# Kernel tuning notes

Measured on AMD Instinct MI355X. Metric: run time of the kernel, lower is better.

The kernel has to match this reference:

```python
import jax, jax.numpy as jnp
import numpy as np

ALPHA = 0.2  # LeakyReLU negative slope


def setup_inputs() -> dict:
    key = jax.random.key(0)
    k_x, k_w, k_a = jax.random.split(key, 3)
    B, N, F_in = 4, 2048, 128
    H, nhid = 4, 32  # out_channel=128, nheads=4
    x = jax.random.normal(k_x, (B, N, F_in), dtype=jnp.float32)
    # per-head projection and attention vector, xavier-ish scale
    W = jax.random.normal(k_w, (H, F_in, nhid), dtype=jnp.float32) * (1.414 * np.sqrt(2.0 / (F_in + nhid))) / np.sqrt(3.0) * np.sqrt(3.0)
    a = jax.random.normal(k_a, (H, 2 * nhid), dtype=jnp.float32) * (1.414 * np.sqrt(2.0 / (2 * nhid + 1)))
    return {"x": x, "W": W, "a": a}


def reference(x, W, a):
    # x: [B,N,F_in], W: [H,F_in,d], a: [H,2d]
    H = W.shape[0]
    d = W.shape[2]
    B, N, _ = x.shape
    Wh = jnp.einsum('bni,hij->bhnj', x, W)          # [B,H,N,d]
    a1 = a[:, :d]                                    # [H,d]
    a2 = a[:, d:]                                    # [H,d]
    Wh1 = jnp.einsum('bhnd,hd->bhn', Wh, a1)         # [B,H,N]
    Wh2 = jnp.einsum('bhnd,hd->bhn', Wh, a2)         # [B,H,N]
    e = Wh1[:, :, :, None] + Wh2[:, :, None, :]      # [B,H,N,N]
    e = jnp.where(e > 0, e, ALPHA * e)               # LeakyReLU
    attn = jax.nn.softmax(e, axis=-1)                # softmax over source nodes
    h = jnp.einsum('bhij,bhjd->bhid', attn, Wh)      # [B,H,N,d]
    h = jax.nn.elu(h)
    # concat heads along feature dim: [B,N,H*d]
    out = jnp.transpose(h, (0, 2, 1, 3)).reshape(B, N, H * d)
    return out
```

## Files before the change

### kernel.cpp

```cpp
#include <hip/hip_runtime.h>


#define LOG2E 1.4426950408889634f
constexpr int Nn = 2048, Fin = 128, Dd = 32;

typedef _Float16 half8 __attribute__((ext_vector_type(8)));
typedef _Float16 half4v __attribute__((ext_vector_type(4)));
typedef float f32x4 __attribute__((ext_vector_type(4)));

__global__ __launch_bounds__(256) void k1_wh(
    const float* __restrict__ x, const float* __restrict__ W,
    const float* __restrict__ a, _Float16* __restrict__ whT,
    float* __restrict__ sArr, float* __restrict__ tArr) {
  int blk = blockIdx.x;
  int bh = blk >> 5, tile = blk & 31;
  int b = bh >> 2, h = bh & 3;
  int tid = threadIdx.x, w = tid >> 6, lane = tid & 63;
  int q = lane >> 4, m = lane & 15;
  int rowbase = tile * 64 + w * 16;

  const float* Wq = W + h * Fin * Dd;
  const float* xb = x + (size_t)(b * Nn + rowbase + m) * Fin;

  f32x4 acc[2];
  acc[0] = (f32x4){0.f, 0.f, 0.f, 0.f};
  acc[1] = (f32x4){0.f, 0.f, 0.f, 0.f};

#pragma unroll
  for (int kt = 0; kt < 4; ++kt) {
    float4 x0 = *(const float4*)(xb + kt * 32 + q * 8);
    float4 x1 = *(const float4*)(xb + kt * 32 + q * 8 + 4);
    float xv[8] = {x0.x, x0.y, x0.z, x0.w, x1.x, x1.y, x1.z, x1.w};
    half8 Ah, Al;
#pragma unroll
    for (int j = 0; j < 8; ++j) {
      _Float16 hi = (_Float16)xv[j];
      Ah[j] = hi;
      Al[j] = (_Float16)(xv[j] - (float)hi);
    }
#pragma unroll
    for (int nt = 0; nt < 2; ++nt) {
      half8 Bh, Bl;
#pragma unroll
      for (int j = 0; j < 8; ++j) {
        float wv = Wq[(kt * 32 + q * 8 + j) * Dd + nt * 16 + m];
        _Float16 hi = (_Float16)wv;
        Bh[j] = hi;
        Bl[j] = (_Float16)(wv - (float)hi);
      }
      acc[nt] = __builtin_amdgcn_mfma_f32_16x16x32_f16(Ah, Bh, acc[nt], 0, 0, 0);
      acc[nt] = __builtin_amdgcn_mfma_f32_16x16x32_f16(Al, Bh, acc[nt], 0, 0, 0);
      acc[nt] = __builtin_amdgcn_mfma_f32_16x16x32_f16(Ah, Bl, acc[nt], 0, 0, 0);
    }
  }

#pragma unroll
  for (int nt = 0; nt < 2; ++nt) {
    int d = nt * 16 + m;
    half4v h4;
#pragma unroll
    for (int r = 0; r < 4; ++r) h4[r] = (_Float16)acc[nt][r];
    *(half4v*)(whT + (size_t)(bh * Dd + d) * Nn + rowbase + q * 4) = h4;
  }

  const float* ah = a + h * 2 * Dd;
  float a1m0 = ah[m], a1m1 = ah[16 + m];
  float a2m0 = ah[Dd + m], a2m1 = ah[Dd + 16 + m];
#pragma unroll
  for (int r = 0; r < 4; ++r) {
    float ps = acc[0][r] * a1m0 + acc[1][r] * a1m1;
    float pt = acc[0][r] * a2m0 + acc[1][r] * a2m1;
#pragma unroll
    for (int off = 1; off < 16; off <<= 1) {
      ps += __shfl_xor(ps, off);
      pt += __shfl_xor(pt, off);
    }
    if (m == 0) {
      sArr[bh * Nn + rowbase + q * 4 + r] = ps;
      tArr[bh * Nn + rowbase + q * 4 + r] = pt;
    }
  }
}

__global__ __launch_bounds__(256) void k3_attn(
    const _Float16* __restrict__ whT, const float* __restrict__ sArr,
    const float* __restrict__ tArr, float* __restrict__ out) {
  __shared__ float smem[4 * 64 * 33 + 256];
  float* Ut = smem;
  float* Vt = smem + 2048;
  float* red = smem + 4096;

  int blk = blockIdx.x;
  int bh = blk >> 5, tile = blk & 31;
  int b = bh >> 2, h = bh & 3;
  int tid = threadIdx.x, w = tid >> 6, lane = tid & 63;
  int q = lane >> 4, m = lane & 15;

  float mx = -1e30f;
  for (int i = tid; i < Nn; i += 256) {
    float t = tArr[bh * Nn + i];
    Ut[i] = LOG2E * t;
    Vt[i] = (0.2f * LOG2E) * t;
    mx = fmaxf(mx, t);
  }
  red[tid] = mx;
  __syncthreads();
  for (int ss = 128; ss > 0; ss >>= 1) {
    if (tid < ss) red[tid] = fmaxf(red[tid], red[tid + ss]);
    __syncthreads();
  }
  float T = red[0];

  float Ar[4], Cr[4];
#pragma unroll
  for (int t = 0; t < 4; ++t) {
    float s = sArr[bh * Nn + tile * 64 + t * 16 + m];
    float e = s + T;
    float mm = fmaxf(e, 0.2f * e);
    Ar[t] = LOG2E * (s - mm);
    Cr[t] = LOG2E * (0.2f * s - mm);
  }

  f32x4 acc[4][2];
#pragma unroll
  for (int t = 0; t < 4; ++t) {
    acc[t][0] = (f32x4){0.f, 0.f, 0.f, 0.f};
    acc[t][1] = (f32x4){0.f, 0.f, 0.f, 0.f};
  }
  float den[4] = {0.f, 0.f, 0.f, 0.f};

  const _Float16* wb = whT + (size_t)bh * Dd * Nn;

  for (int s = 0; s < 16; ++s) {
    int jb = w * 512 + s * 32;
    half8 B0 = *(const half8*)(wb + (size_t)m * Nn + jb + q * 8);
    half8 B1 = *(const half8*)(wb + (size_t)(16 + m) * Nn + jb + q * 8);
    float uu[8], vv[8];
    *(float4*)&uu[0] = *(const float4*)&Ut[jb + q * 8];
    *(float4*)&uu[4] = *(const float4*)&Ut[jb + q * 8 + 4];
    *(float4*)&vv[0] = *(const float4*)&Vt[jb + q * 8];
    *(float4*)&vv[4] = *(const float4*)&Vt[jb + q * 8 + 4];

#pragma unroll
    for (int t = 0; t < 4; ++t) {
      half8 P;
      float ds = 0.f;
#pragma unroll
      for (int k = 0; k < 8; ++k) {
        float p = __builtin_amdgcn_exp2f(fmaxf(Ar[t] + uu[k], Cr[t] + vv[k]));
        ds += p;
        P[k] = (_Float16)p;
      }
      den[t] += ds;
      acc[t][0] = __builtin_amdgcn_mfma_f32_16x16x32_f16(P, B0, acc[t][0], 0, 0, 0);
      acc[t][1] = __builtin_amdgcn_mfma_f32_16x16x32_f16(P, B1, acc[t][1], 0, 0, 0);
    }
  }

#pragma unroll
  for (int t = 0; t < 4; ++t) {
    den[t] += __shfl_xor(den[t], 16);
    den[t] += __shfl_xor(den[t], 32);
  }
  __syncthreads();
  float* redN = smem;
  float* redD = smem + 4 * 64 * 33;
#pragma unroll
  for (int t = 0; t < 4; ++t) {
#pragma unroll
    for (int dh = 0; dh < 2; ++dh)
#pragma unroll
      for (int r = 0; r < 4; ++r)
        redN[(w * 64 + t * 16 + q * 4 + r) * 33 + dh * 16 + m] = acc[t][dh][r];
    if (q == 0) redD[w * 64 + t * 16 + m] = den[t];
  }
  __syncthreads();
  {
    int rl = tid >> 2, dg = (tid & 3) * 8;
    float num[8];
#pragma unroll
    for (int i = 0; i < 8; ++i)
      num[i] = redN[(0 * 64 + rl) * 33 + dg + i] + redN[(1 * 64 + rl) * 33 + dg + i] +
               redN[(2 * 64 + rl) * 33 + dg + i] + redN[(3 * 64 + rl) * 33 + dg + i];
    float dt = redD[rl] + redD[64 + rl] + redD[128 + rl] + redD[192 + rl];
    float rd = 1.0f / dt;
    float* orow = out + (size_t)(b * Nn + tile * 64 + rl) * (4 * Dd) + h * Dd + dg;
#pragma unroll
    for (int i = 0; i < 8; ++i) {
      float hv = num[i] * rd;
      num[i] = hv > 0.f ? hv : (__builtin_amdgcn_exp2f(hv * LOG2E) - 1.0f);
    }
    *(float4*)orow = make_float4(num[0], num[1], num[2], num[3]);
    *((float4*)orow + 1) = make_float4(num[4], num[5], num[6], num[7]);
  }
}

extern "C" void kernel_launch(void* const* d_in, const int* in_sizes, int n_in,
                              void* d_out, int out_size, void* d_ws, size_t ws_size,
                              hipStream_t stream) {
  const float* x = (const float*)d_in[0];
  const float* W = (const float*)d_in[1];
  const float* a = (const float*)d_in[2];
  float* out = (float*)d_out;

  float* wsf = (float*)d_ws;
  float* sArr = wsf;
  float* tArr = sArr + 32768;
  _Float16* whT = (_Float16*)(tArr + 32768);

  k1_wh<<<dim3(512), dim3(256), 0, stream>>>(x, W, a, whT, sArr, tArr);
  k3_attn<<<dim3(512), dim3(256), 0, stream>>>(whT, sArr, tArr, out);
}
```

Before: 84.31 us.

## Factor attention exponentials into per-row and per-column terms with packed fp16 math

Rewrites the leaky-ReLU softmax weights as max(alpha_i*E_j, beta_i*F_j). E_j and F_j are exponentials of the shifted source scores, computed once per block and stored in LDS as fp16. The inner loop then does packed half2 multiplies and max plus fdot2 accumulation instead of one exp2 per element. This removes most transcendental work from the hot loop and halves LDS traffic, at the cost of fp16 precision in the products and possible underflow for large score ranges.

```diff
diff --git a/kernel.cpp b/kernel.cpp
--- a/kernel.cpp
+++ b/kernel.cpp
@@ -6,7 +6,10 @@
 
 typedef _Float16 half8 __attribute__((ext_vector_type(8)));
 typedef _Float16 half4v __attribute__((ext_vector_type(4)));
+typedef _Float16 half2v __attribute__((ext_vector_type(2)));
 typedef float f32x4 __attribute__((ext_vector_type(4)));
+
+union H8 { half2v h2[4]; half8 h8; };
 
 __global__ __launch_bounds__(256) void k1_wh(
     const float* __restrict__ x, const float* __restrict__ W,
@@ -86,9 +89,9 @@
     const _Float16* __restrict__ whT, const float* __restrict__ sArr,
     const float* __restrict__ tArr, float* __restrict__ out) {
   __shared__ float smem[4 * 64 * 33 + 256];
-  float* Ut = smem;
-  float* Vt = smem + 2048;
-  float* red = smem + 4096;
+  _Float16* Ef = (_Float16*)smem;
+  _Float16* Ff = (_Float16*)(smem + 1024);
+  float* red = smem + 2048;
 
   int blk = blockIdx.x;
   int bh = blk >> 5, tile = blk & 31;
@@ -96,12 +99,12 @@
   int tid = threadIdx.x, w = tid >> 6, lane = tid & 63;
   int q = lane >> 4, m = lane & 15;
 
+  float tv[8];
   float mx = -1e30f;
-  for (int i = tid; i < Nn; i += 256) {
-    float t = tArr[bh * Nn + i];
-    Ut[i] = LOG2E * t;
-    Vt[i] = (0.2f * LOG2E) * t;
-    mx = fmaxf(mx, t);
+#pragma unroll
+  for (int k = 0; k < 8; ++k) {
+    tv[k] = tArr[bh * Nn + tid + k * 256];
+    mx = fmaxf(mx, tv[k]);
   }
   red[tid] = mx;
   __syncthreads();
@@ -110,16 +113,25 @@
     __syncthreads();
   }
   float T = red[0];
-
-  float Ar[4], Cr[4];
-#pragma unroll
-  for (int t = 0; t < 4; ++t) {
-    float s = sArr[bh * Nn + tile * 64 + t * 16 + m];
-    float e = s + T;
-    float mm = fmaxf(e, 0.2f * e);
-    Ar[t] = LOG2E * (s - mm);
-    Cr[t] = LOG2E * (0.2f * s - mm);
-  }
+  __syncthreads();
+#pragma unroll
+  for (int k = 0; k < 8; ++k) {
+    float dt = tv[k] - T;
+    Ef[tid + k * 256] = (_Float16)__builtin_amdgcn_exp2f(LOG2E * dt);
+    Ff[tid + k * 256] = (_Float16)__builtin_amdgcn_exp2f(0.2f * LOG2E * dt);
+  }
+
+  half2v aa[4], bb[4];
+#pragma unroll
+  for (int t = 0; t < 4; ++t) {
+    float es = sArr[bh * Nn + tile * 64 + t * 16 + m] + T;
+    float al = __builtin_amdgcn_exp2f(0.8f * LOG2E * fminf(es, 0.f));
+    float be = __builtin_amdgcn_exp2f(-0.8f * LOG2E * fmaxf(es, 0.f));
+    _Float16 ah_ = (_Float16)al, bh_ = (_Float16)be;
+    aa[t] = (half2v){ah_, ah_};
+    bb[t] = (half2v){bh_, bh_};
+  }
+  __syncthreads();
 
   f32x4 acc[4][2];
 #pragma unroll
@@ -128,6 +140,7 @@
     acc[t][1] = (f32x4){0.f, 0.f, 0.f, 0.f};
   }
   float den[4] = {0.f, 0.f, 0.f, 0.f};
+  const half2v ones = (half2v){(_Float16)1.f, (_Float16)1.f};
 
   const _Float16* wb = whT + (size_t)bh * Dd * Nn;
 
@@ -135,25 +148,23 @@
     int jb = w * 512 + s * 32;
     half8 B0 = *(const half8*)(wb + (size_t)m * Nn + jb + q * 8);
     half8 B1 = *(const half8*)(wb + (size_t)(16 + m) * Nn + jb + q * 8);
-    float uu[8], vv[8];
-    *(float4*)&uu[0] = *(const float4*)&Ut[jb + q * 8];
-    *(float4*)&uu[4] = *(const float4*)&Ut[jb + q * 8 + 4];
-    *(float4*)&vv[0] = *(const float4*)&Vt[jb + q * 8];
-    *(float4*)&vv[4] = *(const float4*)&Vt[jb + q * 8 + 4];
+    H8 E, F;
+    E.h8 = *(const half8*)&Ef[jb + q * 8];
+    F.h8 = *(const half8*)&Ff[jb + q * 8];
 
 #pragma unroll
     for (int t = 0; t < 4; ++t) {
-      half8 P;
-      float ds = 0.f;
-#pragma unroll
-      for (int k = 0; k < 8; ++k) {
-        float p = __builtin_amdgcn_exp2f(fmaxf(Ar[t] + uu[k], Cr[t] + vv[k]));
-        ds += p;
-        P[k] = (_Float16)p;
+      H8 P;
+#pragma unroll
+      for (int kk = 0; kk < 4; ++kk) {
+        half2v pe = aa[t] * E.h2[kk];
+        half2v pf = bb[t] * F.h2[kk];
+        half2v p2 = __builtin_elementwise_max(pe, pf);
+        P.h2[kk] = p2;
+        den[t] = __builtin_amdgcn_fdot2(p2, ones, den[t], false);
       }
-      den[t] += ds;
-      acc[t][0] = __builtin_amdgcn_mfma_f32_16x16x32_f16(P, B0, acc[t][0], 0, 0, 0);
-      acc[t][1] = __builtin_amdgcn_mfma_f32_16x16x32_f16(P, B1, acc[t][1], 0, 0, 0);
+      acc[t][0] = __builtin_amdgcn_mfma_f32_16x16x32_f16(P.h8, B0, acc[t][0], 0, 0, 0);
+      acc[t][1] = __builtin_amdgcn_mfma_f32_16x16x32_f16(P.h8, B1, acc[t][1], 0, 0, 0);
     }
   }
 
```

After: 77.38 us, median of 2. 1.09x faster.
